# Kernel tuning notes

Hardware: AMD Instinct MI355X
Metric: run time of the kernel (lower is better)

The kernel has to match this reference:

```python
import jax, jax.numpy as jnp
import numpy as np

N = 100000

def gcn_conv(x, src, dst, W, b, n):
    # x: [N, Fin]; src/dst: [E'] (self-loops already included); W: [Fin, Fout]
    h = x @ W  # [N, Fout]
    deg = jax.ops.segment_sum(jnp.ones_like(dst, dtype=h.dtype), dst, num_segments=n)  # [N]
    dinv = deg ** -0.5  # deg >= 1 due to self-loops
    norm = dinv[src] * dinv[dst]  # [E']
    msg = h[src] * norm[:, None]  # gather + scale, [E', Fout]
    out = jax.ops.segment_sum(msg, dst, num_segments=n)  # scatter-add to targets
    return out + b

def setup_inputs() -> dict:
    key = jax.random.key(0)
    k1, k2, k3, k4, k5, k6 = jax.random.split(key, 6)
    x = jax.random.normal(k1, (N, 128), dtype=jnp.float32)
    edge_index = jax.random.randint(k2, (2, 1600000), 0, N, dtype=jnp.int32)
    W1 = jax.random.normal(k3, (128, 64), dtype=jnp.float32) * 0.1
    b1 = jnp.zeros((64,), dtype=jnp.float32)
    W2 = jax.random.normal(k4, (64, 41), dtype=jnp.float32) * 0.1
    b2 = jnp.zeros((41,), dtype=jnp.float32)
    return {"x": x, "edge_index": edge_index, "W1": W1, "b1": b1, "W2": W2, "b2": b2}

def reference(x, edge_index, W1, b1, W2, b2):
    n = x.shape[0]
    loops = jnp.arange(n, dtype=edge_index.dtype)
    src = jnp.concatenate([edge_index[0], loops])  # add self-loops (PyG gcn_norm default)
    dst = jnp.concatenate([edge_index[1], loops])
    # dropout is identity in eval mode (self.training=False)
    h = gcn_conv(x, src, dst, W1, b1, n)
    h = jax.nn.relu(h)
    out = gcn_conv(h, src, dst, W2, b2, n)
    return out
```

## Files before the change

### kernel.cpp

```cpp
#include <hip/hip_runtime.h>


#define FIN 128
#define F1  64
#define F2  41
#define F2P 48

#define BSH    8
#define BCAP   6144
#define NBMAX  512
#define CHUNK  4096

#define MT 128
#define KC 16

__global__ __launch_bounds__(256) void k_part(
    const int* __restrict__ src, const int* __restrict__ dst,
    int* __restrict__ gcur, int* __restrict__ pairs, int E) {
    __shared__ int hist[NBMAX];
    int tid = threadIdx.x;
    int e0  = blockIdx.x * CHUNK;
    for (int i = tid; i < NBMAX; i += 256) hist[i] = 0;
    __syncthreads();
    for (int j = 0; j < CHUNK / 256; j++) {
        int e = e0 + j * 256 + tid;
        if (e < E) atomicAdd(&hist[dst[e] >> BSH], 1);
    }
    __syncthreads();
    for (int i = tid; i < NBMAX; i += 256) {
        int c = hist[i];
        hist[i] = c ? atomicAdd(&gcur[i], c) : 0;
    }
    __syncthreads();
    for (int j = 0; j < CHUNK / 256; j++) {
        int e = e0 + j * 256 + tid;
        if (e < E) {
            int d = dst[e], s = src[e];
            int b = d >> BSH;
            int pos = atomicAdd(&hist[b], 1);
            if (pos < BCAP) pairs[b * BCAP + pos] = (s << BSH) | (d & 255);
        }
    }
}

__global__ __launch_bounds__(NBMAX) void k_bucketbase(
    const int* __restrict__ gcur, int* __restrict__ bbase,
    int* __restrict__ rowptr, int nbuck, int n, int E) {
    __shared__ int s[NBMAX];
    int t = threadIdx.x;
    int v = (t < nbuck) ? gcur[t] : 0;
    s[t] = v;
    __syncthreads();
    for (int off = 1; off < NBMAX; off <<= 1) {
        int val = s[t];
        int add = (t >= off) ? s[t - off] : 0;
        __syncthreads();
        s[t] = val + add;
        __syncthreads();
    }
    if (t < nbuck) bbase[t] = s[t] - v;
    if (t == 0) rowptr[n] = E;
}

__global__ __launch_bounds__(256) void k_build(
    const int* __restrict__ gcur, const int* __restrict__ bbase,
    const int* __restrict__ pairs, int* __restrict__ adj,
    int* __restrict__ rowptr, float* __restrict__ dinv, int n) {
    __shared__ int lcnt[256];
    __shared__ int lex[256];
    __shared__ int lcur[256];
    __shared__ int ladj[BCAP];
    int tid = threadIdx.x;
    int b   = blockIdx.x;
    int base  = bbase[b];
    int cntb  = gcur[b]; if (cntb > BCAP) cntb = BCAP;
    int node0 = b << BSH;
    const int* pb = pairs + (size_t)b * BCAP;

    lcnt[tid] = 0;
    __syncthreads();
    for (int k = tid; k < cntb; k += 256) atomicAdd(&lcnt[pb[k] & 255], 1);
    __syncthreads();
    int own = lcnt[tid];
    lex[tid] = own;
    __syncthreads();
    for (int off = 1; off < 256; off <<= 1) {
        int val = lex[tid];
        int add = (tid >= off) ? lex[tid - off] : 0;
        __syncthreads();
        lex[tid] = val + add;
        __syncthreads();
    }
    int excl = lex[tid] - own;
    __syncthreads();
    lex[tid]  = excl;
    lcur[tid] = excl;
    __syncthreads();
    for (int k = tid; k < cntb; k += 256) {
        int pk  = pb[k];
        int pos = atomicAdd(&lcur[pk & 255], 1);
        ladj[pos] = pk >> BSH;
    }
    __syncthreads();
    for (int k = tid; k < cntb; k += 256) adj[base + k] = ladj[k];
    int node = node0 + tid;
    if (node < n) {
        rowptr[node] = base + lex[tid];
        dinv[node]   = rsqrtf((float)own + 1.0f);
    }
}

__global__ __launch_bounds__(256) void k_mm1(
    const float* __restrict__ x, const float* __restrict__ W1,
    const float* __restrict__ dinv, float* __restrict__ hs, int n) {
    __shared__ float Ws[FIN * F1];
    __shared__ float As[KC][MT];
    int t  = threadIdx.x;
    int n0 = blockIdx.x * MT;
#pragma unroll
    for (int j = 0; j < 8; j++) {
        int f = j * 256 + t;
        ((float4*)Ws)[f] = ((const float4*)W1)[f];
    }
    int m0 = (t & 15) * 8;
    int c0 = (t >> 4) * 4;
    int m_l = t & 127;
    int kh  = (t >> 7) * 8;
    bool mvalid = (n0 + m_l) < n;
    const float* xrow = x + (size_t)(n0 + m_l) * FIN + kh;
    float acc[8][4] = {};
    for (int kc = 0; kc < FIN; kc += KC) {
        __syncthreads();
        float4 v0 = mvalid ? *(const float4*)(xrow + kc)     : float4{0.f,0.f,0.f,0.f};
        float4 v1 = mvalid ? *(const float4*)(xrow + kc + 4) : float4{0.f,0.f,0.f,0.f};
        As[kh + 0][m_l] = v0.x; As[kh + 1][m_l] = v0.y;
        As[kh + 2][m_l] = v0.z; As[kh + 3][m_l] = v0.w;
        As[kh + 4][m_l] = v1.x; As[kh + 5][m_l] = v1.y;
        As[kh + 6][m_l] = v1.z; As[kh + 7][m_l] = v1.w;
        __syncthreads();
#pragma unroll
        for (int k = 0; k < KC; k++) {
            float4 a0 = *(const float4*)&As[k][m0];
            float4 a1 = *(const float4*)&As[k][m0 + 4];
            float4 w  = *(const float4*)&Ws[(kc + k) * F1 + c0];
            float a[8] = {a0.x, a0.y, a0.z, a0.w, a1.x, a1.y, a1.z, a1.w};
#pragma unroll
            for (int i = 0; i < 8; i++) {
                acc[i][0] += a[i] * w.x;
                acc[i][1] += a[i] * w.y;
                acc[i][2] += a[i] * w.z;
                acc[i][3] += a[i] * w.w;
            }
        }
    }
#pragma unroll
    for (int i = 0; i < 8; i++) {
        int node = n0 + m0 + i;
        if (node < n) {
            float dv = dinv[node];
            float4 o = {acc[i][0] * dv, acc[i][1] * dv, acc[i][2] * dv, acc[i][3] * dv};
            *(float4*)&hs[(size_t)node * F1 + c0] = o;
        }
    }
}

__global__ __launch_bounds__(256) void k_mm2(
    const float* __restrict__ h1, const float* __restrict__ W2,
    const float* __restrict__ dinv, float* __restrict__ hs2, int n) {
    __shared__ float Ws[F1 * F2P];
    __shared__ float As[KC][MT];
    int t  = threadIdx.x;
    int n0 = blockIdx.x * MT;
    for (int idx = t; idx < F1 * F2P; idx += 256) {
        int k = idx / F2P, c = idx - k * F2P;
        Ws[idx] = (c < F2) ? W2[k * F2 + c] : 0.f;
    }
    int m0 = (t & 15) * 8;
    int c0 = (t >> 4) * 4;
    bool compute = (t < 192);
    int m_l = t & 127;
    int kh  = (t >> 7) * 8;
    bool mvalid = (n0 + m_l) < n;
    const float* hrow = h1 + (size_t)(n0 + m_l) * F1 + kh;
    float acc[8][4] = {};
    for (int kc = 0; kc < F1; kc += KC) {
        __syncthreads();
        float4 v0 = mvalid ? *(const float4*)(hrow + kc)     : float4{0.f,0.f,0.f,0.f};
        float4 v1 = mvalid ? *(const float4*)(hrow + kc + 4) : float4{0.f,0.f,0.f,0.f};
        As[kh + 0][m_l] = v0.x; As[kh + 1][m_l] = v0.y;
        As[kh + 2][m_l] = v0.z; As[kh + 3][m_l] = v0.w;
        As[kh + 4][m_l] = v1.x; As[kh + 5][m_l] = v1.y;
        As[kh + 6][m_l] = v1.z; As[kh + 7][m_l] = v1.w;
        __syncthreads();
        if (compute) {
#pragma unroll
            for (int k = 0; k < KC; k++) {
                float4 a0 = *(const float4*)&As[k][m0];
                float4 a1 = *(const float4*)&As[k][m0 + 4];
                float4 w  = *(const float4*)&Ws[(kc + k) * F2P + c0];
                float a[8] = {a0.x, a0.y, a0.z, a0.w, a1.x, a1.y, a1.z, a1.w};
#pragma unroll
                for (int i = 0; i < 8; i++) {
                    acc[i][0] += a[i] * w.x;
                    acc[i][1] += a[i] * w.y;
                    acc[i][2] += a[i] * w.z;
                    acc[i][3] += a[i] * w.w;
                }
            }
        }
    }
    if (compute) {
#pragma unroll
        for (int i = 0; i < 8; i++) {
            int node = n0 + m0 + i;
            if (node < n) {
                float dv = dinv[node];
                float4 o = {acc[i][0] * dv, acc[i][1] * dv, acc[i][2] * dv, acc[i][3] * dv};
                *(float4*)&hs2[(size_t)node * F2P + c0] = o;
            }
        }
    }
}

__global__ __launch_bounds__(256) void k_agg1(
    const int* __restrict__ rowptr, const int* __restrict__ adj,
    const float* __restrict__ hs, const float* __restrict__ dinv,
    const float* __restrict__ b1, float* __restrict__ h1, int n) {
    int node = blockIdx.x * 4 + (threadIdx.x >> 6);
    if (node >= n) return;
    int lane = threadIdx.x & 63;
    int beg = rowptr[node], end = rowptr[node + 1];
    float acc = hs[node * F1 + lane];
    int i = beg;
    for (; i + 4 <= end; i += 4) {
        int s0 = adj[i], s1 = adj[i + 1], s2 = adj[i + 2], s3 = adj[i + 3];
        float a0 = hs[s0 * F1 + lane];
        float a1 = hs[s1 * F1 + lane];
        float a2 = hs[s2 * F1 + lane];
        float a3 = hs[s3 * F1 + lane];
        acc += a0 + a1 + a2 + a3;
    }
    for (; i < end; i++) acc += hs[adj[i] * F1 + lane];
    float v = acc * dinv[node] + b1[lane];
    h1[node * F1 + lane] = v > 0.f ? v : 0.f;
}

__global__ __launch_bounds__(256) void k_agg2(
    const int* __restrict__ rowptr, const int* __restrict__ adj,
    const float* __restrict__ hs2, const float* __restrict__ dinv,
    const float* __restrict__ b2, float* __restrict__ out, int n) {
    int node = blockIdx.x * 4 + (threadIdx.x >> 6);
    if (node >= n) return;
    int lane = threadIdx.x & 63;
    int beg = rowptr[node], end = rowptr[node + 1];
    float acc = (lane < F2) ? hs2[node * F2P + lane] : 0.f;
    int i = beg;
    for (; i + 4 <= end; i += 4) {
        int s0 = adj[i], s1 = adj[i + 1], s2 = adj[i + 2], s3 = adj[i + 3];
        if (lane < F2) {
            acc += hs2[s0 * F2P + lane];
            acc += hs2[s1 * F2P + lane];
            acc += hs2[s2 * F2P + lane];
            acc += hs2[s3 * F2P + lane];
        }
    }
    for (; i < end; i++)
        if (lane < F2) acc += hs2[adj[i] * F2P + lane];
    if (lane < F2) out[node * F2 + lane] = acc * dinv[node] + b2[lane];
}

__global__ void k_zero(int* __restrict__ p, int n) {
    int i = blockIdx.x * blockDim.x + threadIdx.x;
    if (i < n) p[i] = 0;
}

extern "C" void kernel_launch(void* const* d_in, const int* in_sizes, int n_in,
                              void* d_out, int out_size, void* d_ws, size_t ws_size,
                              hipStream_t stream) {
    const float* x  = (const float*)d_in[0];
    const int*   ei = (const int*)d_in[1];
    const float* W1 = (const float*)d_in[2];
    const float* b1 = (const float*)d_in[3];
    const float* W2 = (const float*)d_in[4];
    const float* b2 = (const float*)d_in[5];
    float* out = (float*)d_out;

    const int n = in_sizes[0] / FIN;
    const int E = in_sizes[1] / 2;
    const int* src = ei;
    const int* dst = ei + E;
    const int nbuck   = (n + 255) >> BSH;
    const int nchunks = (E + CHUNK - 1) / CHUNK;
    const int nmm     = (n + MT - 1) / MT;

    char* ws = (char*)d_ws;
    size_t off = 0;
    auto alloc = [&](size_t bytes) {
        void* p = ws + off;
        off = (off + bytes + 511) & ~(size_t)511;
        return p;
    };
    int*   gcur   = (int*)alloc((size_t)NBMAX * 4);
    int*   bbase  = (int*)alloc((size_t)NBMAX * 4);
    int*   pairs  = (int*)alloc((size_t)nbuck * BCAP * 4);
    int*   adj    = (int*)alloc((size_t)E * 4);
    int*   rowptr = (int*)alloc((size_t)(n + 1) * 4);
    float* dinv   = (float*)alloc((size_t)n * 4);
    float* bufHS  = (float*)alloc((size_t)n * F1 * 4);
    float* bufH1  = (float*)alloc((size_t)n * F1 * 4);

    k_zero<<<(NBMAX + 255) / 256, 256, 0, stream>>>(gcur, NBMAX);
    k_part<<<nchunks, 256, 0, stream>>>(src, dst, gcur, pairs, E);
    k_bucketbase<<<1, NBMAX, 0, stream>>>(gcur, bbase, rowptr, nbuck, n, E);
    k_build<<<nbuck, 256, 0, stream>>>(gcur, bbase, pairs, adj, rowptr, dinv, n);

    k_mm1<<<nmm, 256, 0, stream>>>(x, W1, dinv, bufHS, n);
    k_agg1<<<(n + 3) / 4, 256, 0, stream>>>(rowptr, adj, bufHS, dinv, b1, bufH1, n);

    k_mm2<<<nmm, 256, 0, stream>>>(bufH1, W2, dinv, bufHS, n);
    k_agg2<<<(n + 3) / 4, 256, 0, stream>>>(rowptr, adj, bufHS, dinv, b2, out, n);
}
```

Measured before the change: 342.8 us.

## Store pre-scaled features in bf16 for gather-aggregation and cache edges in registers

The matmul kernels now write the dinv-scaled features as bf16 instead of fp32, and both aggregation kernels read bf16 and accumulate in fp32. This halves the bytes moved by the random row gathers that dominate aggregation. Separately, the partition kernel loads each thread's src/dst values into registers once rather than reading dst twice from global memory. The cost is reduced precision of the intermediate features, which may matter against the reference tolerance.

```diff
diff --git a/kernel.cpp b/kernel.cpp
--- a/kernel.cpp
+++ b/kernel.cpp
@@ -13,6 +13,16 @@
 
 #define MT 128
 #define KC 16
+
+__device__ __forceinline__ unsigned short f2bf(float f) {
+    unsigned u = __builtin_bit_cast(unsigned, f);
+    u += 0x7FFFu + ((u >> 16) & 1u);
+    return (unsigned short)(u >> 16);
+}
+__device__ __forceinline__ float bf2f(unsigned short h) {
+    unsigned u = ((unsigned)h) << 16;
+    return __builtin_bit_cast(float, u);
+}
 
 __global__ __launch_bounds__(256) void k_part(
     const int* __restrict__ src, const int* __restrict__ dst,
@@ -20,25 +30,29 @@
     __shared__ int hist[NBMAX];
     int tid = threadIdx.x;
     int e0  = blockIdx.x * CHUNK;
-    for (int i = tid; i < NBMAX; i += 256) hist[i] = 0;
-    __syncthreads();
+    int ds[CHUNK / 256], ss[CHUNK / 256];
+#pragma unroll
     for (int j = 0; j < CHUNK / 256; j++) {
         int e = e0 + j * 256 + tid;
-        if (e < E) atomicAdd(&hist[dst[e] >> BSH], 1);
-    }
+        if (e < E) { ds[j] = dst[e]; ss[j] = src[e]; } else ds[j] = -1;
+    }
+    for (int i = tid; i < NBMAX; i += 256) hist[i] = 0;
+    __syncthreads();
+#pragma unroll
+    for (int j = 0; j < CHUNK / 256; j++)
+        if (ds[j] >= 0) atomicAdd(&hist[ds[j] >> BSH], 1);
     __syncthreads();
     for (int i = tid; i < NBMAX; i += 256) {
         int c = hist[i];
         hist[i] = c ? atomicAdd(&gcur[i], c) : 0;
     }
     __syncthreads();
+#pragma unroll
     for (int j = 0; j < CHUNK / 256; j++) {
-        int e = e0 + j * 256 + tid;
-        if (e < E) {
-            int d = dst[e], s = src[e];
-            int b = d >> BSH;
+        if (ds[j] >= 0) {
+            int b = ds[j] >> BSH;
             int pos = atomicAdd(&hist[b], 1);
-            if (pos < BCAP) pairs[b * BCAP + pos] = (s << BSH) | (d & 255);
+            if (pos < BCAP) pairs[b * BCAP + pos] = (ss[j] << BSH) | (ds[j] & 255);
         }
     }
 }
@@ -112,7 +126,7 @@
 
 __global__ __launch_bounds__(256) void k_mm1(
     const float* __restrict__ x, const float* __restrict__ W1,
-    const float* __restrict__ dinv, float* __restrict__ hs, int n) {
+    const float* __restrict__ dinv, unsigned short* __restrict__ hs, int n) {
     __shared__ float Ws[FIN * F1];
     __shared__ float As[KC][MT];
     int t  = threadIdx.x;
@@ -158,15 +172,39 @@
         int node = n0 + m0 + i;
         if (node < n) {
             float dv = dinv[node];
-            float4 o = {acc[i][0] * dv, acc[i][1] * dv, acc[i][2] * dv, acc[i][3] * dv};
-            *(float4*)&hs[(size_t)node * F1 + c0] = o;
-        }
-    }
+            ushort4 o = { f2bf(acc[i][0] * dv), f2bf(acc[i][1] * dv),
+                          f2bf(acc[i][2] * dv), f2bf(acc[i][3] * dv) };
+            *(ushort4*)&hs[(size_t)node * F1 + c0] = o;
+        }
+    }
+}
+
+__global__ __launch_bounds__(256) void k_agg1(
+    const int* __restrict__ rowptr, const int* __restrict__ adj,
+    const unsigned short* __restrict__ hs, const float* __restrict__ dinv,
+    const float* __restrict__ b1, float* __restrict__ h1, int n) {
+    int node = blockIdx.x * 4 + (threadIdx.x >> 6);
+    if (node >= n) return;
+    int lane = threadIdx.x & 63;
+    int beg = rowptr[node], end = rowptr[node + 1];
+    float acc = bf2f(hs[(size_t)node * F1 + lane]);
+    int i = beg;
+    for (; i + 4 <= end; i += 4) {
+        int s0 = adj[i], s1 = adj[i + 1], s2 = adj[i + 2], s3 = adj[i + 3];
+        float a0 = bf2f(hs[(size_t)s0 * F1 + lane]);
+        float a1 = bf2f(hs[(size_t)s1 * F1 + lane]);
+        float a2 = bf2f(hs[(size_t)s2 * F1 + lane]);
+        float a3 = bf2f(hs[(size_t)s3 * F1 + lane]);
+        acc += a0 + a1 + a2 + a3;
+    }
+    for (; i < end; i++) acc += bf2f(hs[(size_t)adj[i] * F1 + lane]);
+    float v = acc * dinv[node] + b1[lane];
+    h1[(size_t)node * F1 + lane] = v > 0.f ? v : 0.f;
 }
 
 __global__ __launch_bounds__(256) void k_mm2(
     const float* __restrict__ h1, const float* __restrict__ W2,
-    const float* __restrict__ dinv, float* __restrict__ hs2, int n) {
+    const float* __restrict__ dinv, unsigned short* __restrict__ hs2, int n) {
     __shared__ float Ws[F1 * F2P];
     __shared__ float As[KC][MT];
     int t  = threadIdx.x;
@@ -215,58 +253,36 @@
             int node = n0 + m0 + i;
             if (node < n) {
                 float dv = dinv[node];
-                float4 o = {acc[i][0] * dv, acc[i][1] * dv, acc[i][2] * dv, acc[i][3] * dv};
-                *(float4*)&hs2[(size_t)node * F2P + c0] = o;
+                ushort4 o = { f2bf(acc[i][0] * dv), f2bf(acc[i][1] * dv),
+                              f2bf(acc[i][2] * dv), f2bf(acc[i][3] * dv) };
+                *(ushort4*)&hs2[(size_t)node * F2P + c0] = o;
             }
         }
     }
-}
-
-__global__ __launch_bounds__(256) void k_agg1(
-    const int* __restrict__ rowptr, const int* __restrict__ adj,
-    const float* __restrict__ hs, const float* __restrict__ dinv,
-    const float* __restrict__ b1, float* __restrict__ h1, int n) {
-    int node = blockIdx.x * 4 + (threadIdx.x >> 6);
-    if (node >= n) return;
-    int lane = threadIdx.x & 63;
-    int beg = rowptr[node], end = rowptr[node + 1];
-    float acc = hs[node * F1 + lane];
-    int i = beg;
-    for (; i + 4 <= end; i += 4) {
-        int s0 = adj[i], s1 = adj[i + 1], s2 = adj[i + 2], s3 = adj[i + 3];
-        float a0 = hs[s0 * F1 + lane];
-        float a1 = hs[s1 * F1 + lane];
-        float a2 = hs[s2 * F1 + lane];
-        float a3 = hs[s3 * F1 + lane];
-        acc += a0 + a1 + a2 + a3;
-    }
-    for (; i < end; i++) acc += hs[adj[i] * F1 + lane];
-    float v = acc * dinv[node] + b1[lane];
-    h1[node * F1 + lane] = v > 0.f ? v : 0.f;
 }
 
 __global__ __launch_bounds__(256) void k_agg2(
     const int* __restrict__ rowptr, const int* __restrict__ adj,
-    const float* __restrict__ hs2, const float* __restrict__ dinv,
+    const unsigned short* __restrict__ hs2, const float* __restrict__ dinv,
     const float* __restrict__ b2, float* __restrict__ out, int n) {
     int node = blockIdx.x * 4 + (threadIdx.x >> 6);
     if (node >= n) return;
     int lane = threadIdx.x & 63;
     int beg = rowptr[node], end = rowptr[node + 1];
-    float acc = (lane < F2) ? hs2[node * F2P + lane] : 0.f;
+    float acc = (lane < F2) ? bf2f(hs2[(size_t)node * F2P + lane]) : 0.f;
     int i = beg;
     for (; i + 4 <= end; i += 4) {
         int s0 = adj[i], s1 = adj[i + 1], s2 = adj[i + 2], s3 = adj[i + 3];
         if (lane < F2) {
-            acc += hs2[s0 * F2P + lane];
-            acc += hs2[s1 * F2P + lane];
-            acc += hs2[s2 * F2P + lane];
-            acc += hs2[s3 * F2P + lane];
+            acc += bf2f(hs2[(size_t)s0 * F2P + lane]);
+            acc += bf2f(hs2[(size_t)s1 * F2P + lane]);
+            acc += bf2f(hs2[(size_t)s2 * F2P + lane]);
+            acc += bf2f(hs2[(size_t)s3 * F2P + lane]);
         }
     }
     for (; i < end; i++)
-        if (lane < F2) acc += hs2[adj[i] * F2P + lane];
-    if (lane < F2) out[node * F2 + lane] = acc * dinv[node] + b2[lane];
+        if (lane < F2) acc += bf2f(hs2[(size_t)adj[i] * F2P + lane]);
+    if (lane < F2) out[(size_t)node * F2 + lane] = acc * dinv[node] + b2[lane];
 }
 
 __global__ void k_zero(int* __restrict__ p, int n) {
@@ -306,7 +322,7 @@
     int*   adj    = (int*)alloc((size_t)E * 4);
     int*   rowptr = (int*)alloc((size_t)(n + 1) * 4);
     float* dinv   = (float*)alloc((size_t)n * 4);
-    float* bufHS  = (float*)alloc((size_t)n * F1 * 4);
+    unsigned short* bufHS = (unsigned short*)alloc((size_t)n * F1 * 2);
     float* bufH1  = (float*)alloc((size_t)n * F1 * 4);
 
     k_zero<<<(NBMAX + 255) / 256, 256, 0, stream>>>(gcur, NBMAX);
```

Result: faster. 322.0 us (-6.1%).
